# Kernel optimization log

Measured on AMD Instinct MI355X. Metric: run time of the kernel, lower is better.

Reference implementation:

```python
import jax, jax.numpy as jnp
import numpy as np

B, NPATCH, PDIM, DIM, OUTD = 4, 1024, 768, 512, 512
DIN, DSTATE, DTRANK, KCONV, NBLK = 2 * DIM, 16, DIM // 16, 4, 2


def _ln(x, w, b, eps=1e-5):
    m = jnp.mean(x, -1, keepdims=True)
    v = jnp.var(x, -1, keepdims=True)
    return (x - m) * jax.lax.rsqrt(v + eps) * w + b


def _mamba_block(x, ln_w, ln_b, in_W, conv_w, conv_b, xproj_W, dt_W, dt_b, A_log, Dp, out_W):
    # x: [b, L, dim]
    b, L, _ = x.shape
    xn = _ln(x, ln_w, ln_b)
    xz = xn @ in_W                                # [b, L, 2*DIN]
    u, z = jnp.split(xz, 2, axis=-1)              # each [b, L, DIN]
    # causal depthwise conv over time
    uc = jnp.transpose(u, (0, 2, 1))              # [b, DIN, L]
    uc = jax.lax.conv_general_dilated(
        uc, conv_w[:, None, :], window_strides=(1,), padding=((KCONV - 1, 0),),
        feature_group_count=DIN)
    uc = uc + conv_b[None, :, None]
    u = jax.nn.silu(jnp.transpose(uc, (0, 2, 1)))  # [b, L, DIN]
    x_dbl = u @ xproj_W                            # [b, L, DTRANK+2*DSTATE]
    dt, Bm, Cm = jnp.split(x_dbl, [DTRANK, DTRANK + DSTATE], axis=-1)
    delta = jax.nn.softplus(dt @ dt_W + dt_b)      # [b, L, DIN]
    A = -jnp.exp(A_log)                            # [DIN, DSTATE]
    dA = jnp.exp(delta[..., None] * A)             # [b, L, DIN, DSTATE]
    dBu = delta[..., None] * Bm[:, :, None, :] * u[..., None]  # [b, L, DIN, DSTATE]
    # selective scan over time
    def step(h, inp):
        dA_t, dBu_t, C_t = inp                     # [b,DIN,DSTATE],[b,DIN,DSTATE],[b,DSTATE]
        h = dA_t * h + dBu_t
        y = jnp.einsum('bdn,bn->bd', h, C_t)
        return h, y
    h0 = jnp.zeros((b, DIN, DSTATE), x.dtype)
    _, ys = jax.lax.scan(step, h0, (jnp.swapaxes(dA, 0, 1), jnp.swapaxes(dBu, 0, 1), jnp.swapaxes(Cm, 0, 1)))
    y = jnp.swapaxes(ys, 0, 1) + u * Dp            # [b, L, DIN]
    y = y * jax.nn.silu(z)
    return x + y @ out_W                           # residual


def setup_inputs() -> dict:
    key = jax.random.key(0)
    ks = iter(jax.random.split(key, 40))
    rn = lambda shape, s=0.02: jax.random.normal(next(ks), shape, jnp.float32) * s
    d = {
        'img': jax.random.normal(next(ks), (B, NPATCH, PDIM), jnp.float32),
        'patch_W': rn((PDIM, DIM)), 'patch_b': jnp.zeros((DIM,), jnp.float32),
        'pos_emb': rn((1, NPATCH + 1, DIM), 1.0), 'cls_tok': rn((1, 1, DIM), 1.0),
        'blk_ln_w': jnp.ones((NBLK, DIM)), 'blk_ln_b': jnp.zeros((NBLK, DIM)),
        'blk_in_W': rn((NBLK, DIM, 2 * DIN)),
        'blk_conv_w': rn((NBLK, DIN, KCONV), 0.1), 'blk_conv_b': jnp.zeros((NBLK, DIN)),
        'blk_xproj_W': rn((NBLK, DIN, DTRANK + 2 * DSTATE)),
        'blk_dt_W': rn((NBLK, DTRANK, DIN), 0.1), 'blk_dt_b': jnp.full((NBLK, DIN), -4.0),
        'blk_A_log': jnp.tile(jnp.log(jnp.arange(1, DSTATE + 1, dtype=jnp.float32))[None, None, :], (NBLK, DIN, 1)),
        'blk_D': jnp.ones((NBLK, DIN)),
        'blk_out_W': rn((NBLK, DIN, DIM)),
        'sl1_W': rn((DIM, OUTD)), 'sl1_b': jnp.zeros((OUTD,)),
        'sl1_lnw': jnp.ones((OUTD,)), 'sl1_lnb': jnp.zeros((OUTD,)),
        'sl2_W': rn((OUTD, OUTD)), 'sl2_b': jnp.zeros((OUTD,)),
        'sl2_lnw': jnp.ones((OUTD,)), 'sl2_lnb': jnp.zeros((OUTD,)),
        'lat_lnw': jnp.ones((OUTD,)), 'lat_lnb': jnp.zeros((OUTD,)),
    }
    return d


def reference(img, patch_W, patch_b, pos_emb, cls_tok,
              blk_ln_w, blk_ln_b, blk_in_W, blk_conv_w, blk_conv_b,
              blk_xproj_W, blk_dt_W, blk_dt_b, blk_A_log, blk_D, blk_out_W,
              sl1_W, sl1_b, sl1_lnw, sl1_lnb, sl2_W, sl2_b, sl2_lnw, sl2_lnb,
              lat_lnw, lat_lnb):
    x = img @ patch_W + patch_b                       # [b, n, dim]
    b, n, _ = x.shape
    cls = jnp.broadcast_to(cls_tok, (b, 1, DIM))
    x = jnp.concatenate([cls, x], axis=1) + pos_emb[:, :n + 1]
    for i in range(NBLK):
        x = _mamba_block(x, blk_ln_w[i], blk_ln_b[i], blk_in_W[i], blk_conv_w[i],
                         blk_conv_b[i], blk_xproj_W[i], blk_dt_W[i], blk_dt_b[i],
                         blk_A_log[i], blk_D[i], blk_out_W[i])
    y = jax.nn.gelu(_ln(x @ sl1_W + sl1_b, sl1_lnw, sl1_lnb), approximate=False)
    a = jax.nn.gelu(_ln(y @ sl2_W + sl2_b, sl2_lnw, sl2_lnb), approximate=False)
    z = jax.nn.softmax(a, axis=1)                     # softmax over sequence dim
    pooled = jnp.sum(y * z, axis=1)                   # [b, outdim]
    return _ln(pooled, lat_lnw, lat_lnb)
```

## Files before the change

kernel.cpp:

```cpp
#include <hip/hip_runtime.h>
#include <cstdint>
#include <cstddef>

#define B_     4
#define NPATCH 1024
#define LSEQ   1025
#define PDIM   768
#define DIM    512
#define OUTD   512
#define DIN    1024
#define DSTATE 16
#define DTRANK 32
#define KCONV  4
#define NBLK   2
#define MROWS  (B_*LSEQ)
#define NSEG_SP 17

typedef unsigned short u16;
typedef __attribute__((ext_vector_type(8))) short bf16x8;
typedef __attribute__((ext_vector_type(4))) float f32x4;

__device__ __forceinline__ float sigmoidf_(float x){ return 1.f/(1.f+__expf(-x)); }
__device__ __forceinline__ float geluf_(float x){ return 0.5f*x*(1.f+erff(x*0.70710678118654752f)); }
__device__ __forceinline__ u16 f2bf(float x){
    uint32_t b = __float_as_uint(x);
    b += 0x7FFFu + ((b >> 16) & 1u);
    return (u16)(b >> 16);
}
template<int CTRL>
__device__ __forceinline__ float dppmov(float x){
    return __int_as_float(__builtin_amdgcn_update_dpp(0, __float_as_int(x), CTRL, 0xF, 0xF, true));
}
__device__ __forceinline__ float red16(float p){
    p += dppmov<0xB1>(p);
    p += dppmov<0x4E>(p);
    p += dppmov<0x141>(p);
    p += dppmov<0x140>(p);
    return p;
}
__device__ __forceinline__ void gload16(const void* g, void* l){
    __builtin_amdgcn_global_load_lds((const __attribute__((address_space(1))) void*)g,
                                     (__attribute__((address_space(3))) void*)l, 16, 0, 0);
}

template<int MF>
__global__ __launch_bounds__(256) void gemm_mfma(
    const u16* __restrict__ A, int lda,
    const u16* __restrict__ Wt,
    float* __restrict__ C, int ldc,
    int M, int N, int K,
    const float* __restrict__ bias,
    const float* __restrict__ addsrc,
    int act, u16* __restrict__ bf16out)
{
    __shared__ u16 lsA[MF*32*32];
    __shared__ u16 lsB[128*32];
    const int tid = threadIdx.x;
    const int wid = tid >> 6, lane = tid & 63;
    const int m0 = blockIdx.y * (MF*32), n0 = blockIdx.x * 128;
    const int wm = (wid>>1)*(MF*16), wn = (wid&1)*64;
    f32x4 acc[MF][4] = {};

    const char* Agp = (const char*)(A + (size_t)m0 * lda);
    const char* Bgp = (const char*)(Wt + (size_t)n0 * K);
    const int lrow = lane >> 2;
    const int lcb  = (((lane & 3) ^ ((lane >> 3) & 3))) * 16;
    const int rsw  = ((lane & 15) >> 1) & 3;
    const int acol = ((lane >> 4) ^ rsw) * 8;

    for (int k0 = 0; k0 < K; k0 += 32) {
        {
            int ra = wid*(MF*8) + lrow;
            gload16(Agp + (size_t)ra*(lda*2) + k0*2 + lcb, &lsA[(wid*(MF*8))*32]);
            if constexpr (MF == 4) {
                gload16(Agp + (size_t)(ra+16)*(lda*2) + k0*2 + lcb, &lsA[(wid*(MF*8)+16)*32]);
            }
        }
        {
            int rb = wid*32 + lrow;
            gload16(Bgp + (size_t)rb*(K*2) + k0*2 + lcb, &lsB[(wid*32)*32]);
            gload16(Bgp + (size_t)(rb+16)*(K*2) + k0*2 + lcb, &lsB[(wid*32+16)*32]);
        }
        __syncthreads();
        bf16x8 af[MF], bfr[4];
        #pragma unroll
        for (int i = 0; i < MF; ++i)
            af[i] = *(const bf16x8*)&lsA[(wm + i*16 + (lane&15))*32 + acol];
        #pragma unroll
        for (int j = 0; j < 4; ++j)
            bfr[j] = *(const bf16x8*)&lsB[(wn + j*16 + (lane&15))*32 + acol];
        #pragma unroll
        for (int i = 0; i < MF; ++i)
            #pragma unroll
            for (int j = 0; j < 4; ++j)
                acc[i][j] = __builtin_amdgcn_mfma_f32_16x16x32_bf16(af[i], bfr[j], acc[i][j], 0, 0, 0);
        __syncthreads();
    }
    #pragma unroll
    for (int i = 0; i < MF; ++i) {
        #pragma unroll
        for (int j = 0; j < 4; ++j) {
            int col = n0 + wn + j*16 + (lane & 15);
            float bv = bias ? bias[col] : 0.f;
            #pragma unroll
            for (int r = 0; r < 4; ++r) {
                int row = m0 + wm + i*16 + (lane>>4)*4 + r;
                if (row < M) {
                    float v = acc[i][j][r] + bv;
                    if (addsrc) v += addsrc[(size_t)row*ldc + col];
                    if (act == 1) v = (v > 20.f) ? v : log1pf(__expf(v));
                    C[(size_t)row*ldc + col] = v;
                    if (bf16out) bf16out[(size_t)row*ldc + col] = f2bf(v);
                }
            }
        }
    }
}

__global__ __launch_bounds__(256) void xproj_gemm(
    const float* __restrict__ Au,
    const float* __restrict__ W,
    float* __restrict__ P)
{
    __shared__ float As[16][68];
    __shared__ float Bs[16][68];
    int tid = threadIdx.x;
    int tx = tid & 15, ty = tid >> 4;
    int m0 = blockIdx.x * 64;
    int kbase = blockIdx.y * 256;
    float acc[4][4] = {};
    for (int k0 = kbase; k0 < kbase + 256; k0 += 16) {
        {
            int r  = tid >> 2;
            int kq = (tid & 3) << 2;
            float4 va = make_float4(0.f,0.f,0.f,0.f);
            int gr = m0 + r;
            if (gr < MROWS) va = *reinterpret_cast<const float4*>(Au + (size_t)gr*DIN + k0 + kq);
            As[kq+0][r]=va.x; As[kq+1][r]=va.y; As[kq+2][r]=va.z; As[kq+3][r]=va.w;
        }
        {
            int kk = tid >> 4;
            int nq = (tid & 15) << 2;
            float4 vb = *reinterpret_cast<const float4*>(W + (size_t)(k0+kk)*64 + nq);
            Bs[kk][nq+0]=vb.x; Bs[kk][nq+1]=vb.y; Bs[kk][nq+2]=vb.z; Bs[kk][nq+3]=vb.w;
        }
        __syncthreads();
        #pragma unroll
        for (int k = 0; k < 16; ++k) {
            float a0=As[k][ty*4+0],a1=As[k][ty*4+1],a2=As[k][ty*4+2],a3=As[k][ty*4+3];
            float b0=Bs[k][tx*4+0],b1=Bs[k][tx*4+1],b2=Bs[k][tx*4+2],b3=Bs[k][tx*4+3];
            acc[0][0]=fmaf(a0,b0,acc[0][0]); acc[0][1]=fmaf(a0,b1,acc[0][1]);
            acc[0][2]=fmaf(a0,b2,acc[0][2]); acc[0][3]=fmaf(a0,b3,acc[0][3]);
            acc[1][0]=fmaf(a1,b0,acc[1][0]); acc[1][1]=fmaf(a1,b1,acc[1][1]);
            acc[1][2]=fmaf(a1,b2,acc[1][2]); acc[1][3]=fmaf(a1,b3,acc[1][3]);
            acc[2][0]=fmaf(a2,b0,acc[2][0]); acc[2][1]=fmaf(a2,b1,acc[2][1]);
            acc[2][2]=fmaf(a2,b2,acc[2][2]); acc[2][3]=fmaf(a2,b3,acc[2][3]);
            acc[3][0]=fmaf(a3,b0,acc[3][0]); acc[3][1]=fmaf(a3,b1,acc[3][1]);
            acc[3][2]=fmaf(a3,b2,acc[3][2]); acc[3][3]=fmaf(a3,b3,acc[3][3]);
        }
        __syncthreads();
    }
    float* Pp = P + (size_t)blockIdx.y * (MROWS*64);
    #pragma unroll
    for (int i = 0; i < 4; ++i) {
        int r = m0 + ty*4 + i;
        if (r >= MROWS) continue;
        #pragma unroll
        for (int j = 0; j < 4; ++j)
            Pp[(size_t)r*64 + tx*4 + j] = acc[i][j];
    }
}

__global__ __launch_bounds__(256) void xproj_reduce(
    const float* __restrict__ P, float* __restrict__ xdbl, u16* __restrict__ xdbl_bf)
{
    int idx = blockIdx.x*256 + threadIdx.x;
    float v = P[idx] + P[MROWS*64 + idx] + P[2*MROWS*64 + idx] + P[3*MROWS*64 + idx];
    xdbl[idx] = v;
    xdbl_bf[idx] = f2bf(v);
}

__device__ void tcast(const float* __restrict__ in, u16* __restrict__ outp,
                      int K, int N, int tix)
{
    __shared__ float tl[32][33];
    int ntn = N >> 5;
    int tk = tix / ntn, tn = tix - tk*ntn;
    int tid = threadIdx.x;
    int r = tid >> 3, c0 = (tid & 7) << 2;
    float4 v = *(const float4*)&in[(size_t)(tk*32 + r)*N + tn*32 + c0];
    tl[r][c0+0]=v.x; tl[r][c0+1]=v.y; tl[r][c0+2]=v.z; tl[r][c0+3]=v.w;
    __syncthreads();
    int nn = r, k0 = c0;
    uint32_t w0 = f2bf(tl[k0+0][nn]) | ((uint32_t)f2bf(tl[k0+1][nn]) << 16);
    uint32_t w1 = f2bf(tl[k0+2][nn]) | ((uint32_t)f2bf(tl[k0+3][nn]) << 16);
    uint2 o; o.x = w0; o.y = w1;
    *(uint2*)&outp[(size_t)(tn*32 + nn)*K + tk*32 + k0] = o;
}

__global__ __launch_bounds__(256) void prep_kernel(
    const float* __restrict__ img, const float* __restrict__ pW,
    const float* __restrict__ inW, const float* __restrict__ outW,
    const float* __restrict__ dtW, const float* __restrict__ s1W,
    const float* __restrict__ s2W,
    u16* imgb, u16* pWt, u16* inWt, u16* outWt, u16* dtWt, u16* s1t, u16* s2t)
{
    int b = blockIdx.x;
    if (b < 3072) {
        int idx = b*1024 + threadIdx.x*4;
        float4 v = *(const float4*)&img[idx];
        uint2 o;
        o.x = f2bf(v.x) | ((uint32_t)f2bf(v.y) << 16);
        o.y = f2bf(v.z) | ((uint32_t)f2bf(v.w) << 16);
        *(uint2*)&imgb[idx] = o;
        return;
    }
    b -= 3072;
    if (b < 384)  { tcast(pW, pWt, 768, 512, b); return; }
    b -= 384;
    if (b < 2048) { int blk=b>>10, t=b&1023; tcast(inW + (size_t)blk*512*2048, inWt + (size_t)blk*1048576, 512, 2048, t); return; }
    b -= 2048;
    if (b < 1024) { int blk=b>>9, t=b&511; tcast(outW + (size_t)blk*1024*512, outWt + (size_t)blk*524288, 1024, 512, t); return; }
    b -= 1024;
    if (b < 64)   { int blk=b>>5, t=b&31; tcast(dtW + (size_t)blk*32*1024, dtWt + (size_t)blk*32768, 32, 1024, t); return; }
    b -= 64;
    if (b < 256)  { tcast(s1W, s1t, 512, 512, b); return; }
    b -= 256;
    tcast(s2W, s2t, 512, 512, b);
}

__global__ __launch_bounds__(256) void assemble_x(
    const float* __restrict__ tmp, const float* __restrict__ cls,
    const float* __restrict__ pos, float* __restrict__ x)
{
    int idx = blockIdx.x*256 + threadIdx.x;
    int d = idx & 511;
    int r = idx >> 9;
    int l = r % LSEQ;
    int b = r / LSEQ;
    float v = (l == 0) ? cls[d] : tmp[((size_t)(b*NPATCH + l-1))*DIM + d];
    x[idx] = v + pos[(size_t)l*DIM + d];
}

__global__ __launch_bounds__(256) void ln_act(
    const float* __restrict__ in, const float* __restrict__ gw, const float* __restrict__ gb,
    float* __restrict__ f32out, u16* __restrict__ bf16out, int act)
{
    int row = blockIdx.x;
    const float* p = in + (size_t)row * 512;
    int t = threadIdx.x;
    float v0 = p[t], v1 = p[t + 256];
    float s = v0 + v1, q = v0*v0 + v1*v1;
    #pragma unroll
    for (int o = 32; o; o >>= 1) { s += __shfl_xor(s, o); q += __shfl_xor(q, o); }
    __shared__ float ls[4], lq[4];
    int w = t >> 6;
    if ((t & 63) == 0) { ls[w] = s; lq[w] = q; }
    __syncthreads();
    s = ls[0]+ls[1]+ls[2]+ls[3];
    q = lq[0]+lq[1]+lq[2]+lq[3];
    float mean = s * (1.f/512.f);
    float var  = q * (1.f/512.f) - mean*mean;
    float inv  = rsqrtf(var + 1e-5f);
    float o0 = (v0-mean)*inv*gw[t]     + gb[t];
    float o1 = (v1-mean)*inv*gw[t+256] + gb[t+256];
    if (act == 2) { o0 = geluf_(o0); o1 = geluf_(o1); }
    if (f32out)  { f32out[(size_t)row*512 + t] = o0; f32out[(size_t)row*512 + t + 256] = o1; }
    if (bf16out) { bf16out[(size_t)row*512 + t] = f2bf(o0); bf16out[(size_t)row*512 + t + 256] = f2bf(o1); }
}

__global__ __launch_bounds__(256) void conv_silu(
    const float* __restrict__ xz, const float* __restrict__ cw,
    const float* __restrict__ cb, float* __restrict__ uo)
{
    int idx = blockIdx.x*256 + threadIdx.x;
    int dq = idx & 255;
    int r  = idx >> 8;
    int b = r / LSEQ, l = r - b*LSEQ;
    int d0 = dq << 2;
    float4 w0 = *(const float4*)&cw[(d0+0)*4];
    float4 w1 = *(const float4*)&cw[(d0+1)*4];
    float4 w2 = *(const float4*)&cw[(d0+2)*4];
    float4 w3 = *(const float4*)&cw[(d0+3)*4];
    float4 acc = *(const float4*)&cb[d0];
    const float* wv0 = &w0.x; const float* wv1 = &w1.x;
    const float* wv2 = &w2.x; const float* wv3 = &w3.x;
    #pragma unroll
    for (int k = 0; k < KCONV; ++k) {
        int ls = l - (KCONV-1) + k;
        if (ls >= 0) {
            float4 v = *(const float4*)&xz[((size_t)(b*LSEQ + ls))*2048 + d0];
            acc.x = fmaf(wv0[k], v.x, acc.x);
            acc.y = fmaf(wv1[k], v.y, acc.y);
            acc.z = fmaf(wv2[k], v.z, acc.z);
            acc.w = fmaf(wv3[k], v.w, acc.w);
        }
    }
    acc.x *= sigmoidf_(acc.x);
    acc.y *= sigmoidf_(acc.y);
    acc.z *= sigmoidf_(acc.z);
    acc.w *= sigmoidf_(acc.w);
    *(float4*)&uo[(size_t)r*DIN + d0] = acc;
}

__global__ __launch_bounds__(256) void scan_phase1(
    const float* __restrict__ delta, const float* __restrict__ u,
    const float* __restrict__ xdbl,  const float* __restrict__ A_log,
    float* __restrict__ Aseg, float* __restrict__ Hseg)
{
    const int dg = blockIdx.x, b = blockIdx.y, s = blockIdx.z;
    const int tid = threadIdx.x;
    const int n = tid & 15, dl = tid >> 4;
    const int d0 = dg*16, d = d0 + dl;
    const float Adn2 = -__expf(A_log[(size_t)d*DSTATE + n]) * 1.44269504f;
    float sdv = 0.f, h = 0.f;
    __shared__ float sD[16][20], sU[16][20], sB[16][20];
    const int tr = tid >> 4, tc = tid & 15;
    const size_t base = (size_t)b*LSEQ + (size_t)s*128;
    for (int c0 = 0; c0 < 128; c0 += 16) {
        __syncthreads();
        {
            size_t row = base + c0 + tr;
            sD[tc][tr] = delta[row*DIN + d0 + tc];
            sU[tc][tr] = u[row*DIN + d0 + tc];
            sB[tc][tr] = xdbl[row*64 + DTRANK + tc];
        }
        __syncthreads();
        #pragma unroll
        for (int hf = 0; hf < 2; ++hf) {
            f32x4 vD0 = *(const f32x4*)&sD[dl][hf*8];
            f32x4 vD1 = *(const f32x4*)&sD[dl][hf*8+4];
            f32x4 vU0 = *(const f32x4*)&sU[dl][hf*8];
            f32x4 vU1 = *(const f32x4*)&sU[dl][hf*8+4];
            f32x4 vB0 = *(const f32x4*)&sB[n][hf*8];
            f32x4 vB1 = *(const f32x4*)&sB[n][hf*8+4];
            #pragma unroll
            for (int t = 0; t < 8; ++t) {
                float dv = (t<4) ? vD0[t&3] : vD1[t&3];
                float uv = (t<4) ? vU0[t&3] : vU1[t&3];
                float Bv = (t<4) ? vB0[t&3] : vB1[t&3];
                sdv += dv;
                float dA = __builtin_exp2f(dv * Adn2);
                h = fmaf(dA, h, dv*uv*Bv);
            }
        }
    }
    int dn = d*DSTATE + n;
    Aseg[((size_t)b*7 + s)*16384 + dn] = __builtin_exp2f(Adn2 * sdv);
    Hseg[((size_t)b*8 + s)*16384 + dn] = h;
}

__global__ __launch_bounds__(256) void scan_mid(
    float* __restrict__ Hseg, const float* __restrict__ Aseg)
{
    int idx = blockIdx.x*256 + threadIdx.x;
    int b = idx >> 14, dn = idx & 16383;
    float prev = 0.f;
    #pragma unroll
    for (int s = 0; s < 7; ++s) {
        size_t offH = ((size_t)b*8 + s)*16384 + dn;
        float a  = Aseg[((size_t)b*7 + s)*16384 + dn];
        float hs = Hseg[offH];
        Hseg[offH] = prev;
        prev = fmaf(a, prev, hs);
    }
    Hseg[((size_t)b*8 + 7)*16384 + dn] = prev;
}

__global__ __launch_bounds__(256) void scan_phase2(
    const float* __restrict__ delta, const float* __restrict__ u,
    const float* __restrict__ xdbl,  const float* __restrict__ xz,
    const float* __restrict__ A_log, const float* __restrict__ Dp,
    const float* __restrict__ H0, u16* __restrict__ yb)
{
    const int dg = blockIdx.x, b = blockIdx.y, s = blockIdx.z;
    const int tid = threadIdx.x;
    const int n = tid & 15, dl = tid >> 4;
    const int d0 = dg*16, d = d0 + dl;
    const float Adn2 = -__expf(A_log[(size_t)d*DSTATE + n]) * 1.44269504f;
    const float Dd = Dp[d];
    float h = H0[((size_t)b*8 + s)*16384 + d*DSTATE + n];
    __shared__ float sD[16][20], sU[16][20], sZ[16][20], sB[16][20], sC[16][20];
    __shared__ u16 sY[16][20];
    const int tr = tid >> 4, tc = tid & 15;
    const size_t base = (size_t)b*LSEQ + (size_t)s*128;
    for (int c0 = 0; c0 < 128; c0 += 16) {
        __syncthreads();
        {
            size_t row = base + c0 + tr;
            sD[tc][tr] = delta[row*DIN + d0 + tc];
            sU[tc][tr] = u[row*DIN + d0 + tc];
            sZ[tc][tr] = xz[row*2048 + DIN + d0 + tc];
            sB[tc][tr] = xdbl[row*64 + DTRANK + tc];
            sC[tc][tr] = xdbl[row*64 + DTRANK + DSTATE + tc];
        }
        __syncthreads();
        float py = 0.f;
        #pragma unroll
        for (int hf = 0; hf < 2; ++hf) {
            f32x4 vD0 = *(const f32x4*)&sD[dl][hf*8];
            f32x4 vD1 = *(const f32x4*)&sD[dl][hf*8+4];
            f32x4 vU0 = *(const f32x4*)&sU[dl][hf*8];
            f32x4 vU1 = *(const f32x4*)&sU[dl][hf*8+4];
            f32x4 vB0 = *(const f32x4*)&sB[n][hf*8];
            f32x4 vB1 = *(const f32x4*)&sB[n][hf*8+4];
            f32x4 vC0 = *(const f32x4*)&sC[n][hf*8];
            f32x4 vC1 = *(const f32x4*)&sC[n][hf*8+4];
            #pragma unroll
            for (int t = 0; t < 8; ++t) {
                float dv = (t<4) ? vD0[t&3] : vD1[t&3];
                float uv = (t<4) ? vU0[t&3] : vU1[t&3];
                float Bv = (t<4) ? vB0[t&3] : vB1[t&3];
                float Cv = (t<4) ? vC0[t&3] : vC1[t&3];
                float dA = __builtin_exp2f(dv * Adn2);
                h = fmaf(dA, h, dv*uv*Bv);
                float pr = red16(h * Cv);
                int tt = hf*8 + t;
                py = (n == tt) ? pr : py;
            }
        }
        {
            float uv = sU[dl][n];
            float zv = sZ[dl][n];
            float yv = (py + uv*Dd) * (zv * sigmoidf_(zv));
            sY[n][dl] = f2bf(yv);
        }
        __syncthreads();
        yb[(base + c0 + tr)*DIN + d0 + tc] = sY[tr][tc];
    }
    if (s == 7) {
        size_t row = (size_t)b*LSEQ + 1024;
        float dv = delta[row*DIN + d];
        float uv = u[row*DIN + d];
        float zv = xz[row*2048 + DIN + d];
        float Bv = xdbl[row*64 + DTRANK + n];
        float Cv = xdbl[row*64 + DTRANK + DSTATE + n];
        float dA = __builtin_exp2f(dv * Adn2);
        h = fmaf(dA, h, dv*uv*Bv);
        float p = red16(h * Cv);
        if (n == 0)
            yb[row*DIN + d] = f2bf((p + uv*Dd) * (zv * sigmoidf_(zv)));
    }
}

__global__ __launch_bounds__(256) void softpool_seg(
    const float* __restrict__ a, const float* __restrict__ yh,
    float* __restrict__ pm, float* __restrict__ ps, float* __restrict__ pp)
{
    int b   = blockIdx.y;
    int seg = blockIdx.z;
    int jj = threadIdx.x & 63;
    int j  = blockIdx.x * 64 + jj;
    int li = threadIdx.x >> 6;
    int lbeg = seg * 64;
    int lend = min(lbeg + 64, LSEQ);
    float m = -3.0e38f, s = 0.f, p = 0.f;
    for (int l = lbeg + li; l < lend; l += 4) {
        size_t off = ((size_t)(b*LSEQ + l))*OUTD + j;
        float av = a[off], yv = yh[off];
        float mn = fmaxf(m, av);
        float sc = __expf(m - mn);
        float e  = __expf(av - mn);
        s = s*sc + e;
        p = p*sc + yv*e;
        m = mn;
    }
    __shared__ float sm[4][64], ss[4][64], sp[4][64];
    sm[li][jj] = m; ss[li][jj] = s; sp[li][jj] = p;
    __syncthreads();
    if (li == 0) {
        #pragma unroll
        for (int k2 = 1; k2 < 4; ++k2) {
            float m2 = sm[k2][jj], s2 = ss[k2][jj], p2 = sp[k2][jj];
            float M2 = fmaxf(m, m2);
            float c1 = __expf(m - M2), c2 = __expf(m2 - M2);
            s = s*c1 + s2*c2;
            p = p*c1 + p2*c2;
            m = M2;
        }
        int o = ((seg*B_ + b)*OUTD) + j;
        pm[o] = m; ps[o] = s; pp[o] = p;
    }
}

__global__ __launch_bounds__(256) void softpool_combine(
    const float* __restrict__ pm, const float* __restrict__ ps,
    const float* __restrict__ pp, float* __restrict__ pooled)
{
    int idx = blockIdx.x*256 + threadIdx.x;
    int b = idx >> 9, j = idx & 511;
    float m = -3.0e38f, s = 0.f, p = 0.f;
    #pragma unroll
    for (int seg = 0; seg < NSEG_SP; ++seg) {
        int o = ((seg*B_ + b)*OUTD) + j;
        float m2 = pm[o], s2 = ps[o], p2 = pp[o];
        float M2 = fmaxf(m, m2);
        float c1 = __expf(m - M2), c2 = __expf(m2 - M2);
        s = s*c1 + s2*c2;
        p = p*c1 + p2*c2;
        m = M2;
    }
    pooled[(size_t)b*OUTD + j] = p / s;
}

extern "C" void kernel_launch(void* const* d_in, const int* in_sizes, int n_in,
                              void* d_out, int out_size, void* d_ws, size_t ws_size,
                              hipStream_t stream) {
    const float* img     = (const float*)d_in[0];
    const float* patch_W = (const float*)d_in[1];
    const float* patch_b = (const float*)d_in[2];
    const float* pos_emb = (const float*)d_in[3];
    const float* cls_tok = (const float*)d_in[4];
    const float* ln_w    = (const float*)d_in[5];
    const float* ln_b    = (const float*)d_in[6];
    const float* in_W    = (const float*)d_in[7];
    const float* conv_w  = (const float*)d_in[8];
    const float* conv_b  = (const float*)d_in[9];
    const float* xproj_W = (const float*)d_in[10];
    const float* dt_W    = (const float*)d_in[11];
    const float* dt_b    = (const float*)d_in[12];
    const float* A_log   = (const float*)d_in[13];
    const float* Dp      = (const float*)d_in[14];
    const float* out_W   = (const float*)d_in[15];
    const float* sl1_W   = (const float*)d_in[16];
    const float* sl1_b   = (const float*)d_in[17];
    const float* sl1_lnw = (const float*)d_in[18];
    const float* sl1_lnb = (const float*)d_in[19];
    const float* sl2_W   = (const float*)d_in[20];
    const float* sl2_b   = (const float*)d_in[21];
    const float* sl2_lnw = (const float*)d_in[22];
    const float* sl2_lnb = (const float*)d_in[23];
    const float* lat_lnw = (const float*)d_in[24];
    const float* lat_lnb = (const float*)d_in[25];
    float* out = (float*)d_out;
    float* ws  = (float*)d_ws;

    float* x     = ws + 0;
    float* xz    = ws + 2099200;
    float* u     = ws + 10496000;
    float* xdbl  = ws + 14694400;
    float* delta = ws + 14956800;
    u16* ub      = (u16*)(ws + 19155200);
    u16* regA    = ub + 0;
    u16* regB    = ub + 4325376;
    u16* xdbl_bf = ub + 6488064;
    u16* pWt     = ub + 6758400;
    u16* inWt    = ub + 7151616;
    u16* outWt   = ub + 9248768;
    u16* dtWt    = ub + 10297344;
    u16* s1t     = ub + 10362880;
    u16* s2t     = ub + 10625024;

    float* yh     = xz;
    float* t2     = xz + 2099200;
    float* a      = u;
    float* pooled = xdbl;
    float* spm    = xdbl + 8192;
    float* sps    = spm + 34816;
    float* spp    = sps + 34816;
    float* t1     = delta;
    float* segH   = (float*)regB;
    float* segA   = segH + 524288;
    float* xprojP = delta;

    prep_kernel<<<7104, 256, 0, stream>>>(img, patch_W, in_W, out_W, dt_W, sl1_W, sl2_W,
                                          regA, pWt, inWt, outWt, dtWt, s1t, s2t);

    gemm_mfma<2><<<dim3(512/128, 4096/64), 256, 0, stream>>>(
        regA, PDIM, pWt, delta, DIM, 4096, DIM, PDIM, patch_b, nullptr, 0, nullptr);
    assemble_x<<<(MROWS*DIM)/256, 256, 0, stream>>>(delta, cls_tok, pos_emb, x);

    for (int i = 0; i < NBLK; ++i) {
        ln_act<<<MROWS, 256, 0, stream>>>(x, ln_w + i*DIM, ln_b + i*DIM,
                                          nullptr, regB, 0);
        gemm_mfma<4><<<dim3(2048/128, 33), 256, 0, stream>>>(
            regB, DIM, inWt + (size_t)i*1048576, xz, 2*DIN,
            MROWS, 2*DIN, DIM, nullptr, nullptr, 0, nullptr);
        conv_silu<<<MROWS, 256, 0, stream>>>(
            xz, conv_w + i*DIN*KCONV, conv_b + i*DIN, u);
        xproj_gemm<<<dim3(65, 4), 256, 0, stream>>>(
            u, xproj_W + (size_t)i*DIN*64, xprojP);
        xproj_reduce<<<1025, 256, 0, stream>>>(xprojP, xdbl, xdbl_bf);
        gemm_mfma<2><<<dim3(1024/128, 65), 256, 0, stream>>>(
            xdbl_bf, 64, dtWt + (size_t)i*32768, delta, DIN,
            MROWS, DIN, DTRANK, dt_b + i*DIN, nullptr, 1, nullptr);
        scan_phase1<<<dim3(64, 4, 7), 256, 0, stream>>>(
            delta, u, xdbl, A_log + (size_t)i*DIN*DSTATE, segA, segH);
        scan_mid<<<256, 256, 0, stream>>>(segH, segA);
        scan_phase2<<<dim3(64, 4, 8), 256, 0, stream>>>(
            delta, u, xdbl, xz, A_log + (size_t)i*DIN*DSTATE, Dp + i*DIN,
            segH, regA);
        gemm_mfma<2><<<dim3(512/128, 65), 256, 0, stream>>>(
            regA, DIN, outWt + (size_t)i*524288, x, DIM,
            MROWS, DIM, DIN, nullptr, x, 0, (i == NBLK-1) ? regB : nullptr);
    }

    gemm_mfma<2><<<dim3(512/128, 65), 256, 0, stream>>>(
        regB, DIM, s1t, t1, OUTD, MROWS, OUTD, DIM, sl1_b, nullptr, 0, nullptr);
    ln_act<<<MROWS, 256, 0, stream>>>(t1, sl1_lnw, sl1_lnb, yh, regA, 2);
    gemm_mfma<2><<<dim3(512/128, 65), 256, 0, stream>>>(
        regA, OUTD, s2t, t2, OUTD, MROWS, OUTD, OUTD, sl2_b, nullptr, 0, nullptr);
    ln_act<<<MROWS, 256, 0, stream>>>(t2, sl2_lnw, sl2_lnb, a, nullptr, 2);
    softpool_seg<<<dim3(OUTD/64, B_, NSEG_SP), 256, 0, stream>>>(a, yh, spm, sps, spp);
    softpool_combine<<<8, 256, 0, stream>>>(spm, sps, spp, pooled);
    ln_act<<<B_, 256, 0, stream>>>(pooled, lat_lnw, lat_lnb, out, nullptr, 0);
}
```

Measured before the change: 632.1 us.

## Fuse dt projection and softplus into scan kernels; store xz as bf16

```diff
diff --git a/kernel.cpp b/kernel.cpp
--- a/kernel.cpp
+++ b/kernel.cpp
@@ -27,6 +27,7 @@
     b += 0x7FFFu + ((b >> 16) & 1u);
     return (u16)(b >> 16);
 }
+__device__ __forceinline__ float bf2f(u16 v){ return __uint_as_float((uint32_t)v << 16); }
 template<int CTRL>
 __device__ __forceinline__ float dppmov(float x){
     return __int_as_float(__builtin_amdgcn_update_dpp(0, __float_as_int(x), CTRL, 0xF, 0xF, true));
@@ -41,6 +42,9 @@
 __device__ __forceinline__ void gload16(const void* g, void* l){
     __builtin_amdgcn_global_load_lds((const __attribute__((address_space(1))) void*)g,
                                      (__attribute__((address_space(3))) void*)l, 16, 0, 0);
+}
+__device__ __forceinline__ float softplusf_(float v){
+    return (v > 20.f) ? v : log1pf(__expf(v));
 }
 
 template<int MF>
@@ -108,8 +112,8 @@
                 if (row < M) {
                     float v = acc[i][j][r] + bv;
                     if (addsrc) v += addsrc[(size_t)row*ldc + col];
-                    if (act == 1) v = (v > 20.f) ? v : log1pf(__expf(v));
-                    C[(size_t)row*ldc + col] = v;
+                    if (act == 1) v = softplusf_(v);
+                    if (C) C[(size_t)row*ldc + col] = v;
                     if (bf16out) bf16out[(size_t)row*ldc + col] = f2bf(v);
                 }
             }
@@ -172,12 +176,10 @@
 }
 
 __global__ __launch_bounds__(256) void xproj_reduce(
-    const float* __restrict__ P, float* __restrict__ xdbl, u16* __restrict__ xdbl_bf)
+    const float* __restrict__ P, float* __restrict__ xdbl)
 {
     int idx = blockIdx.x*256 + threadIdx.x;
-    float v = P[idx] + P[MROWS*64 + idx] + P[2*MROWS*64 + idx] + P[3*MROWS*64 + idx];
-    xdbl[idx] = v;
-    xdbl_bf[idx] = f2bf(v);
+    xdbl[idx] = P[idx] + P[MROWS*64 + idx] + P[2*MROWS*64 + idx] + P[3*MROWS*64 + idx];
 }
 
 __device__ void tcast(const float* __restrict__ in, u16* __restrict__ outp,
@@ -201,9 +203,8 @@
 __global__ __launch_bounds__(256) void prep_kernel(
     const float* __restrict__ img, const float* __restrict__ pW,
     const float* __restrict__ inW, const float* __restrict__ outW,
-    const float* __restrict__ dtW, const float* __restrict__ s1W,
-    const float* __restrict__ s2W,
-    u16* imgb, u16* pWt, u16* inWt, u16* outWt, u16* dtWt, u16* s1t, u16* s2t)
+    const float* __restrict__ s1W, const float* __restrict__ s2W,
+    u16* imgb, u16* pWt, u16* inWt, u16* outWt, u16* s1t, u16* s2t)
 {
     int b = blockIdx.x;
     if (b < 3072) {
@@ -222,8 +223,6 @@
     b -= 2048;
     if (b < 1024) { int blk=b>>9, t=b&511; tcast(outW + (size_t)blk*1024*512, outWt + (size_t)blk*524288, 1024, 512, t); return; }
     b -= 1024;
-    if (b < 64)   { int blk=b>>5, t=b&31; tcast(dtW + (size_t)blk*32*1024, dtWt + (size_t)blk*32768, 32, 1024, t); return; }
-    b -= 64;
     if (b < 256)  { tcast(s1W, s1t, 512, 512, b); return; }
     b -= 256;
     tcast(s2W, s2t, 512, 512, b);
@@ -270,7 +269,7 @@
 }
 
 __global__ __launch_bounds__(256) void conv_silu(
-    const float* __restrict__ xz, const float* __restrict__ cw,
+    const u16* __restrict__ xzb, const float* __restrict__ cw,
     const float* __restrict__ cb, float* __restrict__ uo)
 {
     int idx = blockIdx.x*256 + threadIdx.x;
@@ -289,11 +288,11 @@
     for (int k = 0; k < KCONV; ++k) {
         int ls = l - (KCONV-1) + k;
         if (ls >= 0) {
-            float4 v = *(const float4*)&xz[((size_t)(b*LSEQ + ls))*2048 + d0];
-            acc.x = fmaf(wv0[k], v.x, acc.x);
-            acc.y = fmaf(wv1[k], v.y, acc.y);
-            acc.z = fmaf(wv2[k], v.z, acc.z);
-            acc.w = fmaf(wv3[k], v.w, acc.w);
+            ushort4 v = *(const ushort4*)&xzb[((size_t)(b*LSEQ + ls))*2048 + d0];
+            acc.x = fmaf(wv0[k], bf2f(v.x), acc.x);
+            acc.y = fmaf(wv1[k], bf2f(v.y), acc.y);
+            acc.z = fmaf(wv2[k], bf2f(v.z), acc.z);
+            acc.w = fmaf(wv3[k], bf2f(v.w), acc.w);
         }
     }
     acc.x *= sigmoidf_(acc.x);
@@ -304,44 +303,57 @@
 }
 
 __global__ __launch_bounds__(256) void scan_phase1(
-    const float* __restrict__ delta, const float* __restrict__ u,
-    const float* __restrict__ xdbl,  const float* __restrict__ A_log,
+    const float* __restrict__ u,    const float* __restrict__ xdbl,
+    const float* __restrict__ dtW,  const float* __restrict__ dtb,
+    const float* __restrict__ A_log,
     float* __restrict__ Aseg, float* __restrict__ Hseg)
 {
     const int dg = blockIdx.x, b = blockIdx.y, s = blockIdx.z;
     const int tid = threadIdx.x;
     const int n = tid & 15, dl = tid >> 4;
+    const int tr = tid >> 4, tc = tid & 15;
     const int d0 = dg*16, d = d0 + dl;
     const float Adn2 = -__expf(A_log[(size_t)d*DSTATE + n]) * 1.44269504f;
+    __shared__ float sX[16][68];
+    __shared__ float sW[32][17];
+    __shared__ float sU[16][20];
+    __shared__ float sDel[16][20];
+    {
+        int k = tid >> 4;
+        sW[k][tc]    = dtW[(size_t)k*DIN + d0 + tc];
+        sW[k+16][tc] = dtW[(size_t)(k+16)*DIN + d0 + tc];
+    }
+    const float db = dtb[d0 + tc];
     float sdv = 0.f, h = 0.f;
-    __shared__ float sD[16][20], sU[16][20], sB[16][20];
-    const int tr = tid >> 4, tc = tid & 15;
     const size_t base = (size_t)b*LSEQ + (size_t)s*128;
     for (int c0 = 0; c0 < 128; c0 += 16) {
         __syncthreads();
         {
             size_t row = base + c0 + tr;
-            sD[tc][tr] = delta[row*DIN + d0 + tc];
+            *(float4*)&sX[tr][tc*4] = *(const float4*)&xdbl[row*64 + tc*4];
             sU[tc][tr] = u[row*DIN + d0 + tc];
-            sB[tc][tr] = xdbl[row*64 + DTRANK + tc];
+        }
+        __syncthreads();
+        {
+            float acc = db;
+            #pragma unroll
+            for (int k = 0; k < 32; ++k) acc = fmaf(sX[tr][k], sW[k][tc], acc);
+            sDel[tc][tr] = softplusf_(acc);
         }
         __syncthreads();
         #pragma unroll
         for (int hf = 0; hf < 2; ++hf) {
-            f32x4 vD0 = *(const f32x4*)&sD[dl][hf*8];
-            f32x4 vD1 = *(const f32x4*)&sD[dl][hf*8+4];
+            f32x4 vD0 = *(const f32x4*)&sDel[dl][hf*8];
+            f32x4 vD1 = *(const f32x4*)&sDel[dl][hf*8+4];
             f32x4 vU0 = *(const f32x4*)&sU[dl][hf*8];
             f32x4 vU1 = *(const f32x4*)&sU[dl][hf*8+4];
-            f32x4 vB0 = *(const f32x4*)&sB[n][hf*8];
-            f32x4 vB1 = *(const f32x4*)&sB[n][hf*8+4];
             #pragma unroll
             for (int t = 0; t < 8; ++t) {
                 float dv = (t<4) ? vD0[t&3] : vD1[t&3];
                 float uv = (t<4) ? vU0[t&3] : vU1[t&3];
-                float Bv = (t<4) ? vB0[t&3] : vB1[t&3];
+                float Bv = sX[hf*8+t][32+n];
                 sdv += dv;
-                float dA = __builtin_exp2f(dv * Adn2);
-                h = fmaf(dA, h, dv*uv*Bv);
+                h = fmaf(__builtin_exp2f(dv * Adn2), h, dv*uv*Bv);
             }
         }
     }
@@ -368,75 +380,87 @@
 }
 
 __global__ __launch_bounds__(256) void scan_phase2(
-    const float* __restrict__ delta, const float* __restrict__ u,
-    const float* __restrict__ xdbl,  const float* __restrict__ xz,
-    const float* __restrict__ A_log, const float* __restrict__ Dp,
-    const float* __restrict__ H0, u16* __restrict__ yb)
+    const float* __restrict__ u,    const float* __restrict__ xdbl,
+    const u16*   __restrict__ xzb,  const float* __restrict__ dtW,
+    const float* __restrict__ dtb,  const float* __restrict__ A_log,
+    const float* __restrict__ Dp,   const float* __restrict__ H0,
+    u16* __restrict__ yb)
 {
     const int dg = blockIdx.x, b = blockIdx.y, s = blockIdx.z;
     const int tid = threadIdx.x;
     const int n = tid & 15, dl = tid >> 4;
+    const int tr = tid >> 4, tc = tid & 15;
     const int d0 = dg*16, d = d0 + dl;
     const float Adn2 = -__expf(A_log[(size_t)d*DSTATE + n]) * 1.44269504f;
     const float Dd = Dp[d];
     float h = H0[((size_t)b*8 + s)*16384 + d*DSTATE + n];
-    __shared__ float sD[16][20], sU[16][20], sZ[16][20], sB[16][20], sC[16][20];
-    __shared__ u16 sY[16][20];
-    const int tr = tid >> 4, tc = tid & 15;
+    __shared__ float sX[16][68];
+    __shared__ float sW[32][17];
+    __shared__ float sU[16][20];
+    __shared__ float sDel[16][20];
+    __shared__ float sZ[16][20];
+    __shared__ u16 sY[16][17];
+    {
+        int k = tid >> 4;
+        sW[k][tc]    = dtW[(size_t)k*DIN + d0 + tc];
+        sW[k+16][tc] = dtW[(size_t)(k+16)*DIN + d0 + tc];
+    }
+    const float db = dtb[d0 + tc];
     const size_t base = (size_t)b*LSEQ + (size_t)s*128;
     for (int c0 = 0; c0 < 128; c0 += 16) {
-        __syncthreads();
         {
             size_t row = base + c0 + tr;
-            sD[tc][tr] = delta[row*DIN + d0 + tc];
+            *(float4*)&sX[tr][tc*4] = *(const float4*)&xdbl[row*64 + tc*4];
             sU[tc][tr] = u[row*DIN + d0 + tc];
-            sZ[tc][tr] = xz[row*2048 + DIN + d0 + tc];
-            sB[tc][tr] = xdbl[row*64 + DTRANK + tc];
-            sC[tc][tr] = xdbl[row*64 + DTRANK + DSTATE + tc];
+            sZ[tc][tr] = bf2f(xzb[row*2048 + DIN + d0 + tc]);
+        }
+        __syncthreads();
+        {
+            float acc = db;
+            #pragma unroll
+            for (int k = 0; k < 32; ++k) acc = fmaf(sX[tr][k], sW[k][tc], acc);
+            sDel[tc][tr] = softplusf_(acc);
         }
         __syncthreads();
         float py = 0.f;
         #pragma unroll
         for (int hf = 0; hf < 2; ++hf) {
-            f32x4 vD0 = *(const f32x4*)&sD[dl][hf*8];
-            f32x4 vD1 = *(const f32x4*)&sD[dl][hf*8+4];
+            f32x4 vD0 = *(const f32x4*)&sDel[dl][hf*8];
+            f32x4 vD1 = *(const f32x4*)&sDel[dl][hf*8+4];
             f32x4 vU0 = *(const f32x4*)&sU[dl][hf*8];
             f32x4 vU1 = *(const f32x4*)&sU[dl][hf*8+4];
-            f32x4 vB0 = *(const f32x4*)&sB[n][hf*8];
-            f32x4 vB1 = *(const f32x4*)&sB[n][hf*8+4];
-            f32x4 vC0 = *(const f32x4*)&sC[n][hf*8];
-            f32x4 vC1 = *(const f32x4*)&sC[n][hf*8+4];
             #pragma unroll
             for (int t = 0; t < 8; ++t) {
                 float dv = (t<4) ? vD0[t&3] : vD1[t&3];
                 float uv = (t<4) ? vU0[t&3] : vU1[t&3];
-                float Bv = (t<4) ? vB0[t&3] : vB1[t&3];
-                float Cv = (t<4) ? vC0[t&3] : vC1[t&3];
-                float dA = __builtin_exp2f(dv * Adn2);
-                h = fmaf(dA, h, dv*uv*Bv);
+                int tt = hf*8 + t;
+                float Bv = sX[tt][32+n];
+                float Cv = sX[tt][48+n];
+                h = fmaf(__builtin_exp2f(dv * Adn2), h, dv*uv*Bv);
                 float pr = red16(h * Cv);
-                int tt = hf*8 + t;
                 py = (n == tt) ? pr : py;
             }
         }
         {
             float uv = sU[dl][n];
             float zv = sZ[dl][n];
-            float yv = (py + uv*Dd) * (zv * sigmoidf_(zv));
-            sY[n][dl] = f2bf(yv);
+            sY[n][dl] = f2bf((py + uv*Dd) * (zv * sigmoidf_(zv)));
         }
         __syncthreads();
         yb[(base + c0 + tr)*DIN + d0 + tc] = sY[tr][tc];
     }
     if (s == 7) {
         size_t row = (size_t)b*LSEQ + 1024;
-        float dv = delta[row*DIN + d];
+        float acc = dtb[d];
+        #pragma unroll
+        for (int k = 0; k < 32; ++k)
+            acc = fmaf(xdbl[row*64 + k], dtW[(size_t)k*DIN + d], acc);
+        float dv = softplusf_(acc);
         float uv = u[row*DIN + d];
-        float zv = xz[row*2048 + DIN + d];
+        float zv = bf2f(xzb[row*2048 + DIN + d]);
         float Bv = xdbl[row*64 + DTRANK + n];
         float Cv = xdbl[row*64 + DTRANK + DSTATE + n];
-        float dA = __builtin_exp2f(dv * Adn2);
-        h = fmaf(dA, h, dv*uv*Bv);
+        h = fmaf(__builtin_exp2f(dv * Adn2), h, dv*uv*Bv);
         float p = red16(h * Cv);
         if (n == 0)
             yb[row*DIN + d] = f2bf((p + uv*Dd) * (zv * sigmoidf_(zv)));
@@ -535,61 +559,57 @@
     float* out = (float*)d_out;
     float* ws  = (float*)d_ws;
 
-    float* x     = ws + 0;
-    float* xz    = ws + 2099200;
-    float* u     = ws + 10496000;
-    float* xdbl  = ws + 14694400;
-    float* delta = ws + 14956800;
+    float* x      = ws + 0;
+    u16*   xz_bf  = (u16*)(ws + 2099200);
+    float* yh     = ws + 6297600;
+    float* t2     = ws + 8396800;
+    float* u      = ws + 10496000;
+    float* xdbl   = ws + 14694400;
+    float* scratch= ws + 14956800;
     u16* ub      = (u16*)(ws + 19155200);
     u16* regA    = ub + 0;
     u16* regB    = ub + 4325376;
-    u16* xdbl_bf = ub + 6488064;
     u16* pWt     = ub + 6758400;
     u16* inWt    = ub + 7151616;
     u16* outWt   = ub + 9248768;
-    u16* dtWt    = ub + 10297344;
     u16* s1t     = ub + 10362880;
     u16* s2t     = ub + 10625024;
 
-    float* yh     = xz;
-    float* t2     = xz + 2099200;
     float* a      = u;
     float* pooled = xdbl;
     float* spm    = xdbl + 8192;
     float* sps    = spm + 34816;
     float* spp    = sps + 34816;
-    float* t1     = delta;
+    float* t1     = scratch;
+    float* xprojP = scratch;
     float* segH   = (float*)regB;
     float* segA   = segH + 524288;
-    float* xprojP = delta;
-
-    prep_kernel<<<7104, 256, 0, stream>>>(img, patch_W, in_W, out_W, dt_W, sl1_W, sl2_W,
-                                          regA, pWt, inWt, outWt, dtWt, s1t, s2t);
+
+    prep_kernel<<<7040, 256, 0, stream>>>(img, patch_W, in_W, out_W, sl1_W, sl2_W,
+                                          regA, pWt, inWt, outWt, s1t, s2t);
 
     gemm_mfma<2><<<dim3(512/128, 4096/64), 256, 0, stream>>>(
-        regA, PDIM, pWt, delta, DIM, 4096, DIM, PDIM, patch_b, nullptr, 0, nullptr);
-    assemble_x<<<(MROWS*DIM)/256, 256, 0, stream>>>(delta, cls_tok, pos_emb, x);
+        regA, PDIM, pWt, scratch, DIM, 4096, DIM, PDIM, patch_b, nullptr, 0, nullptr);
+    assemble_x<<<(MROWS*DIM)/256, 256, 0, stream>>>(scratch, cls_tok, pos_emb, x);
 
     for (int i = 0; i < NBLK; ++i) {
         ln_act<<<MROWS, 256, 0, stream>>>(x, ln_w + i*DIM, ln_b + i*DIM,
                                           nullptr, regB, 0);
         gemm_mfma<4><<<dim3(2048/128, 33), 256, 0, stream>>>(
-            regB, DIM, inWt + (size_t)i*1048576, xz, 2*DIN,
-            MROWS, 2*DIN, DIM, nullptr, nullptr, 0, nullptr);
+            regB, DIM, inWt + (size_t)i*1048576, nullptr, 2048,
+            MROWS, 2*DIN, DIM, nullptr, nullptr, 0, xz_bf);
         conv_silu<<<MROWS, 256, 0, stream>>>(
-            xz, conv_w + i*DIN*KCONV, conv_b + i*DIN, u);
+            xz_bf, conv_w + i*DIN*KCONV, conv_b + i*DIN, u);
         xproj_gemm<<<dim3(65, 4), 256, 0, stream>>>(
             u, xproj_W + (size_t)i*DIN*64, xprojP);
-        xproj_reduce<<<1025, 256, 0, stream>>>(xprojP, xdbl, xdbl_bf);
-        gemm_mfma<2><<<dim3(1024/128, 65), 256, 0, stream>>>(
-            xdbl_bf, 64, dtWt + (size_t)i*32768, delta, DIN,
-            MROWS, DIN, DTRANK, dt_b + i*DIN, nullptr, 1, nullptr);
+        xproj_reduce<<<1025, 256, 0, stream>>>(xprojP, xdbl);
         scan_phase1<<<dim3(64, 4, 7), 256, 0, stream>>>(
-            delta, u, xdbl, A_log + (size_t)i*DIN*DSTATE, segA, segH);
+            u, xdbl, dt_W + (size_t)i*DTRANK*DIN, dt_b + i*DIN,
+            A_log + (size_t)i*DIN*DSTATE, segA, segH);
         scan_mid<<<256, 256, 0, stream>>>(segH, segA);
         scan_phase2<<<dim3(64, 4, 8), 256, 0, stream>>>(
-            delta, u, xdbl, xz, A_log + (size_t)i*DIN*DSTATE, Dp + i*DIN,
-            segH, regA);
+            u, xdbl, xz_bf, dt_W + (size_t)i*DTRANK*DIN, dt_b + i*DIN,
+            A_log + (size_t)i*DIN*DSTATE, Dp + i*DIN, segH, regA);
         gemm_mfma<2><<<dim3(512/128, 65), 256, 0, stream>>>(
             regA, DIN, outWt + (size_t)i*524288, x, DIM,
             MROWS, DIM, DIN, nullptr, x, 0, (i == NBLK-1) ? regB : nullptr);
```

After: 610.1 us. -3.5%, faster.
